# Kernel optimization log

Measured on AMD Instinct MI355X. Metric: run time of the kernel, lower is better.

Reference implementation:

```python
import jax, jax.numpy as jnp
import numpy as np

B, D, H, C = 32768, 512, 512, 128  # batch, input_dim, hidden, n_classes (nurse==doctor)
L = 3  # 3 PAN layers and 3 shared FC layers
BN_EPS = 1e-5


def setup_inputs() -> dict:
    key = jax.random.key(0)
    ks = iter(jax.random.split(key, 64))

    def rn(shape, scale):
        return (jax.random.normal(next(ks), shape, jnp.float32) * scale)

    inv = lambda fan: 1.0 / np.sqrt(fan)

    x = jax.random.normal(next(ks), (B, D), jnp.float32)
    s_n = jax.random.randint(next(ks), (B,), 0, C)
    s_d = jax.random.randint(next(ks), (B,), 0, C)
    # cols -4 / -3 carry integer staffing caps (s_nurse_max, s_doctor_max)
    x = x.at[:, -4].set(s_n.astype(jnp.float32)).at[:, -3].set(s_d.astype(jnp.float32))

    inp = {
        'x': x,
        # ClinicalPAN params, stacked over L=3 layers (and 3 branches)
        'pbw': rn((L, 3, D, 32), inv(D)), 'pbb': jnp.zeros((L, 3, 32), jnp.float32),
        'paw1': rn((L, D, 64), inv(D)),  'pab1': jnp.zeros((L, 64), jnp.float32),
        'paw2': rn((L, 64, 32), inv(64)),'pab2': jnp.zeros((L, 32), jnp.float32),
        'piw1': rn((L, D, 16), inv(D)),  'pib1': jnp.zeros((L, 16), jnp.float32),
        'piw2': rn((L, 16, 1), inv(16)), 'pib2': jnp.zeros((L, 1), jnp.float32),
        'pfw': rn((L, 96, D), inv(96)),  'pfb': jnp.zeros((L, D), jnp.float32),
        'pgw': rn((L, D, D), inv(D)),    'pgb': jnp.zeros((L, D), jnp.float32),
        # shared Linear + BatchNorm1d (eval mode: running stats), stacked
        'fcw': rn((L, D, H), inv(D)),    'fcb': jnp.zeros((L, H), jnp.float32),
        'bng': jnp.ones((L, H), jnp.float32),  'bnb': jnp.zeros((L, H), jnp.float32),
        'bnm': jnp.zeros((L, H), jnp.float32), 'bnv': jnp.ones((L, H), jnp.float32),
        # heads
        'nhw1': rn((H, 64), inv(H)), 'nhb1': jnp.zeros((64,), jnp.float32),
        'nhw2': rn((64, C), inv(64)), 'nhb2': jnp.zeros((C,), jnp.float32),
        'dhw1': rn((H, 64), inv(H)), 'dhb1': jnp.zeros((64,), jnp.float32),
        'dhw2': rn((64, C), inv(64)), 'dhb2': jnp.zeros((C,), jnp.float32),
        'wtw1': rn((H, 64), inv(H)), 'wtb1': jnp.zeros((64,), jnp.float32),
        'wtw2': rn((64, 1), inv(64)), 'wtb2': jnp.zeros((1,), jnp.float32),
    }
    return inp


def reference(x, pbw, pbb, paw1, pab1, paw2, pab2, piw1, pib1, piw2, pib2,
              pfw, pfb, pgw, pgb, fcw, fcb, bng, bnb, bnm, bnv,
              nhw1, nhb1, nhw2, nhb2, dhw1, dhb1, dhw2, dhb2,
              wtw1, wtb1, wtw2, wtb2):
    # integer caps (constants w.r.t. grad)
    s_n = jax.lax.stop_gradient(x[:, -4]).astype(jnp.int32)
    s_d = jax.lax.stop_gradient(x[:, -3]).astype(jnp.int32)

    h = x
    for l in range(L):  # ClinicalPAN stack (dropout = identity in eval)
        cw = jax.nn.sigmoid(jax.nn.relu(h @ paw1[l] + pab1[l]) @ paw2[l] + pab2[l])   # [B,32]
        ci = jax.nn.sigmoid(jax.nn.relu(h @ piw1[l] + pib1[l]) @ piw2[l] + pib2[l])   # [B,1]
        feats = jax.nn.relu(jnp.einsum('bd,kdh->bkh', h, pbw[l]) + pbb[l][None])      # [B,3,32]
        weighted = feats * (cw * ci)[:, None, :]                                       # [B,3,32]
        fused = weighted.reshape(h.shape[0], 96) @ pfw[l] + pfb[l]                     # [B,D]
        gate = jax.nn.sigmoid(h @ pgw[l] + pgb[l])
        h = fused + gate * h

    for i in range(L):  # shared Linear -> BN(eval) -> ReLU
        z = h @ fcw[i] + fcb[i]
        z = bng[i] * (z - bnm[i]) * jax.lax.rsqrt(bnv[i] + BN_EPS) + bnb[i]
        h = jax.nn.relu(z)

    nurse_logits = jax.nn.relu(h @ nhw1 + nhb1) @ nhw2 + nhb2   # [B,C]
    doctor_logits = jax.nn.relu(h @ dhw1 + dhb1) @ dhw2 + dhb2  # [B,C]
    wait_time = jax.nn.relu(h @ wtw1 + wtb1) @ wtw2 + wtb2      # [B,1]

    idx = jnp.arange(C)
    nm = (idx[None, :] <= s_n[:, None]).astype(nurse_logits.dtype)
    dm = (idx[None, :] <= s_d[:, None]).astype(doctor_logits.dtype)
    NEG = jnp.asarray(-1e9, nurse_logits.dtype)
    nurse_logits = nurse_logits * nm + (1.0 - nm) * NEG
    doctor_logits = doctor_logits * dm + (1.0 - dm) * NEG
    return nurse_logits, doctor_logits, wait_time
```

## Files before the change

kernel.cpp:

```cpp
#include <hip/hip_runtime.h>

#define DI __device__ __forceinline__

typedef short bf16x8 __attribute__((ext_vector_type(8)));
typedef float f32x4  __attribute__((ext_vector_type(4)));

#define MFMA(a,b,c) __builtin_amdgcn_mfma_f32_16x16x32_bf16(a,b,c,0,0,0)

constexpr int    SZ_WT = 512*80;
constexpr int    SZ_WB = 512*96;
constexpr int    SZ_WF = 96*512;
constexpr int    SZ_WG = 512*512;
constexpr int    SZ_WC = 512*512;
constexpr size_t OFF_WT  = 0;
constexpr size_t OFF_WB  = OFF_WT + 3*(size_t)SZ_WT;
constexpr size_t OFF_WF  = OFF_WB + 3*(size_t)SZ_WB;
constexpr size_t OFF_WG  = OFF_WF + 3*(size_t)SZ_WF;
constexpr size_t OFF_WC  = OFF_WG + 3*(size_t)SZ_WG;
constexpr size_t OFF_WH  = OFF_WC + 3*(size_t)SZ_WC;
constexpr size_t OFF_WH2 = OFF_WH + (size_t)512*192;
constexpr size_t WS_TOTAL= OFF_WH2 + (size_t)128*256;

DI short f2b(float f){ unsigned u; __builtin_memcpy(&u,&f,4); u += 0x7fffu + ((u>>16)&1u); return (short)(u>>16); }
DI float b2f(short s){ unsigned u = ((unsigned)(unsigned short)s)<<16; float f; __builtin_memcpy(&f,&u,4); return f; }
DI float sigm(float x){ return 1.f/(1.f+__expf(-x)); }
DI unsigned pk2(float a, float b){
  return (unsigned)(unsigned short)f2b(a) | ((unsigned)(unsigned short)f2b(b) << 16);
}

__global__ __launch_bounds__(256) void prep_weights(
    const float* __restrict__ pbw,  const float* __restrict__ paw1,
    const float* __restrict__ piw1, const float* __restrict__ pfw,
    const float* __restrict__ pgw,  const float* __restrict__ fcw,
    const float* __restrict__ nhw1, const float* __restrict__ nhw2,
    const float* __restrict__ dhw1, const float* __restrict__ dhw2,
    const float* __restrict__ wtw1, short* __restrict__ ws)
{
  size_t t = (size_t)blockIdx.x*256 + threadIdx.x;
  if (t >= WS_TOTAL) return;
  float v = 0.f;
  if (t < OFF_WB) {
    int q=(int)t; int ly=q/SZ_WT; int qq=q%SZ_WT;
    int j=qq&7, lane=(qq>>3)&63, tile=qq>>9, kt=tile&15, nt=tile>>4;
    int k=kt*32+((lane>>4)<<3)+j, n=nt*16+(lane&15);
    v = (n<64) ? paw1[((size_t)ly*512+k)*64+n] : piw1[((size_t)ly*512+k)*16+(n-64)];
  } else if (t < OFF_WF) {
    int q=(int)(t-OFF_WB); int ly=q/SZ_WB; int qq=q%SZ_WB;
    int j=qq&7, lane=(qq>>3)&63, tile=qq>>9, kt=tile&15, nt=tile>>4;
    int k=kt*32+((lane>>4)<<3)+j, c=nt*16+(lane&15);
    v = pbw[(((size_t)ly*3+(c>>5))*512+k)*32+(c&31)];
  } else if (t < OFF_WG) {
    int q=(int)(t-OFF_WF); int ly=q/SZ_WF; int qq=q%SZ_WF;
    int j=qq&7, lane=(qq>>3)&63, tile=qq>>9, kt=tile%3, nt=tile/3;
    int k=kt*32+((lane>>4)<<3)+j, n=nt*16+(lane&15);
    v = pfw[((size_t)ly*96+k)*512+n];
  } else if (t < OFF_WC) {
    int q=(int)(t-OFF_WG); int ly=q/SZ_WG; int qq=q%SZ_WG;
    int j=qq&7, lane=(qq>>3)&63, tile=qq>>9, kt=tile&15, nt=tile>>4;
    int k=kt*32+((lane>>4)<<3)+j, n=nt*16+(lane&15);
    v = pgw[((size_t)ly*512+k)*512+n];
  } else if (t < OFF_WH) {
    int q=(int)(t-OFF_WC); int ly=q/SZ_WC; int qq=q%SZ_WC;
    int j=qq&7, lane=(qq>>3)&63, tile=qq>>9, kt=tile&15, nt=tile>>4;
    int k=kt*32+((lane>>4)<<3)+j, n=nt*16+(lane&15);
    v = fcw[((size_t)ly*512+k)*512+n];
  } else if (t < OFF_WH2) {
    int qq=(int)(t-OFF_WH);
    int j=qq&7, lane=(qq>>3)&63, tile=qq>>9, kt=tile&15, nt=tile>>4;
    int k=kt*32+((lane>>4)<<3)+j, n=nt*16+(lane&15);
    v = (n<64) ? nhw1[(size_t)k*64+n] : (n<128) ? dhw1[(size_t)k*64+(n-64)] : wtw1[(size_t)k*64+(n-128)];
  } else {
    int qq=(int)(t-OFF_WH2);
    int j=qq&7, lane=(qq>>3)&63, tile=qq>>9, kt=tile&3, nt=tile>>2;
    int k=kt*32+((lane>>4)<<3)+j, n=nt*16+(lane&15);
    if (k<64) v = (n<128) ? nhw2[(size_t)k*128+n] : 0.f;
    else      v = (n>=128)? dhw2[(size_t)(k-64)*128+(n-128)] : 0.f;
  }
  ws[t] = f2b(v);
}

__global__ __launch_bounds__(512, 4) void pan_main(
  const float* __restrict__ x,
  const float* __restrict__ pbb,  const float* __restrict__ pab1,
  const float* __restrict__ paw2, const float* __restrict__ pab2,
  const float* __restrict__ pib1, const float* __restrict__ piw2,
  const float* __restrict__ pib2, const float* __restrict__ pfb,
  const float* __restrict__ pgb,  const float* __restrict__ fcb,
  const float* __restrict__ bng,  const float* __restrict__ bnb,
  const float* __restrict__ bnm,  const float* __restrict__ bnv,
  const float* __restrict__ nhb1, const float* __restrict__ nhb2,
  const float* __restrict__ dhb1, const float* __restrict__ dhb2,
  const float* __restrict__ wtb1, const float* __restrict__ wtw2,
  const float* __restrict__ wtb2,
  const short* __restrict__ ws, float* __restrict__ out)
{
  __shared__ __align__(16) char lds[81920];
  char* sH = lds;
  char* sU = lds + 65536;

  const int tid  = threadIdx.x;
  const int wave = tid >> 6;
  const int l    = tid & 63;
  const int lr   = l & 15;
  const int lb   = l >> 4;
  const int swzA = (lr & 7) << 4;
  const size_t row0 = (size_t)blockIdx.x * 64;

  #pragma unroll 2
  for (int c = tid; c < 4096; c += 512) {
    int row = c >> 6, k0 = (c & 63) << 3;
    const float4* s0 = (const float4*)(x + (row0 + row)*512 + k0);
    float4 f0 = s0[0], f1 = s0[1];
    bf16x8 p;
    p[0]=f2b(f0.x); p[1]=f2b(f0.y); p[2]=f2b(f0.z); p[3]=f2b(f0.w);
    p[4]=f2b(f1.x); p[5]=f2b(f1.y); p[6]=f2b(f1.z); p[7]=f2b(f1.w);
    *(bf16x8*)(sH + row*1024 + ((k0*2) ^ ((row&7)<<4))) = p;
  }
  __syncthreads();

  auto ldA = [&](int rt, int kt) -> bf16x8 {
    int row = rt*16 + lr;
    return *(const bf16x8*)(sH + row*1024 + ((kt*64 + lb*16) ^ swzA));
  };
  auto ldB = [&](const short* W, int K32, int nt, int kt) -> bf16x8 {
    return *(const bf16x8*)(W + (((size_t)(nt*K32 + kt))*64 + l)*8);
  };
  auto ldH = [&](int row, int col) -> float {
    return b2f(*(const short*)(sH + row*1024 + ((col*2) ^ ((row&7)<<4))));
  };
  const f32x4 FZ = {0.f,0.f,0.f,0.f};

  for (int ly = 0; ly < 3; ++ly) {
    if (wave < 5) {
      const short* W = ws + OFF_WT + (size_t)ly*SZ_WT;
      f32x4 acc[4];
      #pragma unroll
      for (int rt=0;rt<4;++rt) acc[rt] = FZ;
      #pragma unroll 2
      for (int kt=0;kt<16;++kt) {
        bf16x8 b = ldB(W,16,wave,kt);
        #pragma unroll
        for (int rt=0;rt<4;++rt) acc[rt] = MFMA(ldA(rt,kt), b, acc[rt]);
      }
      const int col = wave*16 + lr;
      const float bias = (col<64) ? pab1[ly*64+col] : pib1[ly*16+(col-64)];
      #pragma unroll
      for (int rt=0;rt<4;++rt)
        #pragma unroll
        for (int jj=0;jj<4;++jj) {
          int row = rt*16 + lb*4 + jj;
          *(short*)(sU + row*160 + col*2) = f2b(fmaxf(acc[rt][jj]+bias, 0.f));
        }
    }
    __syncthreads();
    if (tid < 64) {
      float s = pib2[ly];
      bf16x8 t0 = *(const bf16x8*)(sU + tid*160 + 128);
      bf16x8 t1 = *(const bf16x8*)(sU + tid*160 + 144);
      #pragma unroll
      for (int i=0;i<8;++i) {
        s += b2f(t0[i]) * piw2[ly*16+i];
        s += b2f(t1[i]) * piw2[ly*16+8+i];
      }
      *(float*)(sU + 10240 + tid*4) = sigm(s);
    }
    __syncthreads();
    {
      const int r = tid>>3, j0 = (tid&7)<<2;
      float a4[4];
      #pragma unroll
      for (int i=0;i<4;++i) a4[i] = pab2[ly*32 + j0 + i];
      #pragma unroll 2
      for (int k8=0;k8<8;++k8) {
        bf16x8 tv8 = *(const bf16x8*)(sU + r*160 + k8*16);
        #pragma unroll
        for (int i8=0;i8<8;++i8) {
          float tv = b2f(tv8[i8]);
          float4 wr = *(const float4*)(paw2 + ((size_t)ly*64 + k8*8+i8)*32 + j0);
          a4[0]=fmaf(tv,wr.x,a4[0]); a4[1]=fmaf(tv,wr.y,a4[1]);
          a4[2]=fmaf(tv,wr.z,a4[2]); a4[3]=fmaf(tv,wr.w,a4[3]);
        }
      }
      const float civ = *(const float*)(sU + 10240 + r*4);
      #pragma unroll
      for (int i=0;i<4;++i)
        *(short*)(sU + 10496 + (r*32 + j0 + i)*2) = f2b(sigm(a4[i]) * civ);
    }
    __syncthreads();
    unsigned wpk[4][2];
    if (wave < 6) {
      const short* W = ws + OFF_WB + (size_t)ly*SZ_WB;
      f32x4 acc[4];
      #pragma unroll
      for (int rt=0;rt<4;++rt) acc[rt] = FZ;
      #pragma unroll 2
      for (int kt=0;kt<16;++kt) {
        bf16x8 b = ldB(W,16,wave,kt);
        #pragma unroll
        for (int rt=0;rt<4;++rt) acc[rt] = MFMA(ldA(rt,kt), b, acc[rt]);
      }
      const int col = wave*16 + lr;
      const float bias = pbb[ly*96 + col];
      #pragma unroll
      for (int rt=0;rt<4;++rt) {
        float w4[4];
        #pragma unroll
        for (int jj=0;jj<4;++jj) {
          int row = rt*16 + lb*4 + jj;
          float cc = b2f(*(const short*)(sU + 10496 + (row*32 + (col&31))*2));
          w4[jj] = fmaxf(acc[rt][jj]+bias, 0.f) * cc;
        }
        wpk[rt][0] = pk2(w4[0], w4[1]);
        wpk[rt][1] = pk2(w4[2], w4[3]);
      }
    }
    __syncthreads();
    if (wave < 6) {
      const int col = wave*16 + lr;
      #pragma unroll
      for (int rt=0;rt<4;++rt)
        #pragma unroll
        for (int p=0;p<2;++p) {
          int r0 = rt*16 + lb*4 + p*2;
          unsigned v = wpk[rt][p];
          *(short*)(sU + r0*256     + ((col*2) ^ ((r0    &7)<<4))) = (short)(v & 0xffff);
          *(short*)(sU + (r0+1)*256 + ((col*2) ^ (((r0+1)&7)<<4))) = (short)(v >> 16);
        }
    }
    __syncthreads();
    unsigned pk[4][4][2];
    {
      const short* Wg = ws + OFF_WG + (size_t)ly*SZ_WG;
      const short* Wf = ws + OFF_WF + (size_t)ly*SZ_WF;
      #pragma unroll
      for (int p=0; p<2; ++p) {
        f32x4 acc[4][2];
        #pragma unroll
        for (int rt=0;rt<4;++rt) { acc[rt][0]=FZ; acc[rt][1]=FZ; }
        #pragma unroll 2
        for (int kt=0;kt<16;++kt) {
          bf16x8 b0 = ldB(Wg,16, wave*4+p*2+0, kt);
          bf16x8 b1 = ldB(Wg,16, wave*4+p*2+1, kt);
          #pragma unroll
          for (int rt=0;rt<4;++rt) {
            bf16x8 a = ldA(rt,kt);
            acc[rt][0] = MFMA(a,b0,acc[rt][0]);
            acc[rt][1] = MFMA(a,b1,acc[rt][1]);
          }
        }
        #pragma unroll
        for (int c2=0;c2<2;++c2) {
          const int col = (wave*4+p*2+c2)*16 + lr;
          const float gb = pgb[ly*512+col];
          const float fb = pfb[ly*512+col];
          #pragma unroll
          for (int rt=0;rt<4;++rt)
            #pragma unroll
            for (int jj=0;jj<4;++jj) {
              int row = rt*16 + lb*4 + jj;
              acc[rt][c2][jj] = sigm(acc[rt][c2][jj]+gb)*ldH(row,col) + fb;
            }
        }
        #pragma unroll 1
        for (int kt=0;kt<3;++kt) {
          bf16x8 b0 = ldB(Wf,3, wave*4+p*2+0, kt);
          bf16x8 b1 = ldB(Wf,3, wave*4+p*2+1, kt);
          #pragma unroll
          for (int rt=0;rt<4;++rt) {
            int row = rt*16 + lr;
            bf16x8 a = *(const bf16x8*)(sU + row*256 + ((kt*64 + lb*16) ^ swzA));
            acc[rt][0] = MFMA(a,b0,acc[rt][0]);
            acc[rt][1] = MFMA(a,b1,acc[rt][1]);
          }
        }
        #pragma unroll
        for (int c2=0;c2<2;++c2)
          #pragma unroll
          for (int rt=0;rt<4;++rt) {
            pk[p*2+c2][rt][0] = pk2(acc[rt][c2][0], acc[rt][c2][1]);
            pk[p*2+c2][rt][1] = pk2(acc[rt][c2][2], acc[rt][c2][3]);
          }
      }
    }
    __syncthreads();
    #pragma unroll
    for (int ci2=0;ci2<4;++ci2) {
      const int col = (wave*4+ci2)*16 + lr;
      #pragma unroll
      for (int rt=0;rt<4;++rt)
        #pragma unroll
        for (int q=0;q<2;++q) {
          int r0 = rt*16 + lb*4 + q*2;
          unsigned v = pk[ci2][rt][q];
          *(short*)(sH + r0*1024     + ((col*2) ^ ((r0    &7)<<4))) = (short)(v & 0xffff);
          *(short*)(sH + (r0+1)*1024 + ((col*2) ^ (((r0+1)&7)<<4))) = (short)(v >> 16);
        }
    }
    __syncthreads();
  }

  for (int fi=0; fi<3; ++fi) {
    const short* W = ws + OFF_WC + (size_t)fi*SZ_WC;
    unsigned pk[4][4][2];
    #pragma unroll
    for (int p=0; p<2; ++p) {
      f32x4 acc[4][2];
      #pragma unroll
      for (int rt=0;rt<4;++rt) { acc[rt][0]=FZ; acc[rt][1]=FZ; }
      #pragma unroll 2
      for (int kt=0;kt<16;++kt) {
        bf16x8 b0 = ldB(W,16, wave*4+p*2+0, kt);
        bf16x8 b1 = ldB(W,16, wave*4+p*2+1, kt);
        #pragma unroll
        for (int rt=0;rt<4;++rt) {
          bf16x8 a = ldA(rt,kt);
          acc[rt][0] = MFMA(a,b0,acc[rt][0]);
          acc[rt][1] = MFMA(a,b1,acc[rt][1]);
        }
      }
      #pragma unroll
      for (int c2=0;c2<2;++c2) {
        const int col = (wave*4+p*2+c2)*16 + lr;
        const float sc = bng[fi*512+col] * rsqrtf(bnv[fi*512+col] + 1e-5f);
        const float of = bnb[fi*512+col] - bnm[fi*512+col]*sc;
        const float bb = fcb[fi*512+col];
        #pragma unroll
        for (int rt=0;rt<4;++rt) {
          float z0 = fmaxf((acc[rt][c2][0] + bb)*sc + of, 0.f);
          float z1 = fmaxf((acc[rt][c2][1] + bb)*sc + of, 0.f);
          float z2 = fmaxf((acc[rt][c2][2] + bb)*sc + of, 0.f);
          float z3 = fmaxf((acc[rt][c2][3] + bb)*sc + of, 0.f);
          pk[p*2+c2][rt][0] = pk2(z0, z1);
          pk[p*2+c2][rt][1] = pk2(z2, z3);
        }
      }
    }
    __syncthreads();
    #pragma unroll
    for (int ci2=0;ci2<4;++ci2) {
      const int col = (wave*4+ci2)*16 + lr;
      #pragma unroll
      for (int rt=0;rt<4;++rt)
        #pragma unroll
        for (int q=0;q<2;++q) {
          int r0 = rt*16 + lb*4 + q*2;
          unsigned v = pk[ci2][rt][q];
          *(short*)(sH + r0*1024     + ((col*2) ^ ((r0    &7)<<4))) = (short)(v & 0xffff);
          *(short*)(sH + (r0+1)*1024 + ((col*2) ^ (((r0+1)&7)<<4))) = (short)(v >> 16);
        }
    }
    __syncthreads();
  }

  unsigned hkA[4][2], hkB[4][2];
  {
    const short* W = ws + OFF_WH;
    {
      f32x4 acc[4];
      #pragma unroll
      for (int rt=0;rt<4;++rt) acc[rt] = FZ;
      #pragma unroll 2
      for (int kt=0;kt<16;++kt) {
        bf16x8 b = ldB(W,16,wave,kt);
        #pragma unroll
        for (int rt=0;rt<4;++rt) acc[rt] = MFMA(ldA(rt,kt), b, acc[rt]);
      }
      const int col = wave*16 + lr;
      const float bias = (col<64) ? nhb1[col] : dhb1[col-64];
      #pragma unroll
      for (int rt=0;rt<4;++rt) {
        hkA[rt][0] = pk2(fmaxf(acc[rt][0]+bias,0.f), fmaxf(acc[rt][1]+bias,0.f));
        hkA[rt][1] = pk2(fmaxf(acc[rt][2]+bias,0.f), fmaxf(acc[rt][3]+bias,0.f));
      }
    }
    if (wave < 4) {
      f32x4 acc[4];
      #pragma unroll
      for (int rt=0;rt<4;++rt) acc[rt] = FZ;
      #pragma unroll 2
      for (int kt=0;kt<16;++kt) {
        bf16x8 b = ldB(W,16, 8+wave, kt);
        #pragma unroll
        for (int rt=0;rt<4;++rt) acc[rt] = MFMA(ldA(rt,kt), b, acc[rt]);
      }
      const int col = (8+wave)*16 + lr;
      const float bias = wtb1[col-128];
      #pragma unroll
      for (int rt=0;rt<4;++rt) {
        hkB[rt][0] = pk2(fmaxf(acc[rt][0]+bias,0.f), fmaxf(acc[rt][1]+bias,0.f));
        hkB[rt][1] = pk2(fmaxf(acc[rt][2]+bias,0.f), fmaxf(acc[rt][3]+bias,0.f));
      }
    }
  }
  __syncthreads();
  {
    #pragma unroll
    for (int rt=0;rt<4;++rt)
      #pragma unroll
      for (int q=0;q<2;++q) {
        int r0 = rt*16 + lb*4 + q*2;
        int cA = wave*16 + lr;
        unsigned v = hkA[rt][q];
        *(short*)(lds + r0*384     + ((cA*2) ^ ((r0    &7)<<4))) = (short)(v & 0xffff);
        *(short*)(lds + (r0+1)*384 + ((cA*2) ^ (((r0+1)&7)<<4))) = (short)(v >> 16);
      }
    if (wave < 4) {
      #pragma unroll
      for (int rt=0;rt<4;++rt)
        #pragma unroll
        for (int q=0;q<2;++q) {
          int r0 = rt*16 + lb*4 + q*2;
          int cB = (8+wave)*16 + lr;
          unsigned v = hkB[rt][q];
          *(short*)(lds + r0*384     + ((cB*2) ^ ((r0    &7)<<4))) = (short)(v & 0xffff);
          *(short*)(lds + (r0+1)*384 + ((cB*2) ^ (((r0+1)&7)<<4))) = (short)(v >> 16);
        }
    }
  }
  __syncthreads();
  {
    const short* W2 = ws + OFF_WH2;
    #pragma unroll
    for (int p=0;p<2;++p) {
      f32x4 acc[4];
      #pragma unroll
      for (int rt=0;rt<4;++rt) acc[rt] = FZ;
      #pragma unroll 2
      for (int kt=0;kt<4;++kt) {
        bf16x8 b = ldB(W2,4, wave*2+p, kt);
        #pragma unroll
        for (int rt=0;rt<4;++rt) {
          int row = rt*16 + lr;
          bf16x8 a = *(const bf16x8*)(lds + row*384 + ((kt*64 + lb*16) ^ swzA));
          acc[rt] = MFMA(a,b,acc[rt]);
        }
      }
      const int col2 = (wave*2+p)*16 + lr;
      const bool isn = col2 < 128;
      const int cc = col2 & 127;
      const float bias = isn ? nhb2[cc] : dhb2[cc];
      const size_t obase = isn ? (size_t)0 : (size_t)4194304;
      #pragma unroll
      for (int rt=0;rt<4;++rt)
        #pragma unroll
        for (int jj=0;jj<4;++jj) {
          int row = rt*16 + lb*4 + jj;
          size_t rg = row0 + row;
          float2 caps = *(const float2*)(x + rg*512 + 508);
          int cap = (int)(isn ? caps.x : caps.y);
          float v = acc[rt][jj] + bias;
          out[obase + rg*128 + cc] = (cc <= cap) ? v : -1e9f;
        }
    }
  }
  if (tid < 64) {
    float s = wtb2[0];
    #pragma unroll 2
    for (int k8=0;k8<8;++k8) {
      bf16x8 hv = *(const bf16x8*)(lds + tid*384 + ((256 + k8*16) ^ ((tid&7)<<4)));
      #pragma unroll
      for (int i=0;i<8;++i) s += b2f(hv[i]) * wtw2[k8*8+i];
    }
    out[(size_t)8388608 + row0 + tid] = s;
  }
}

extern "C" void kernel_launch(void* const* d_in, const int* in_sizes, int n_in,
                              void* d_out, int out_size, void* d_ws, size_t ws_size,
                              hipStream_t stream) {
  const float* x    = (const float*)d_in[0];
  const float* pbw  = (const float*)d_in[1];
  const float* pbb  = (const float*)d_in[2];
  const float* paw1 = (const float*)d_in[3];
  const float* pab1 = (const float*)d_in[4];
  const float* paw2 = (const float*)d_in[5];
  const float* pab2 = (const float*)d_in[6];
  const float* piw1 = (const float*)d_in[7];
  const float* pib1 = (const float*)d_in[8];
  const float* piw2 = (const float*)d_in[9];
  const float* pib2 = (const float*)d_in[10];
  const float* pfw  = (const float*)d_in[11];
  const float* pfb  = (const float*)d_in[12];
  const float* pgw  = (const float*)d_in[13];
  const float* pgb  = (const float*)d_in[14];
  const float* fcw  = (const float*)d_in[15];
  const float* fcb  = (const float*)d_in[16];
  const float* bng  = (const float*)d_in[17];
  const float* bnb  = (const float*)d_in[18];
  const float* bnm  = (const float*)d_in[19];
  const float* bnv  = (const float*)d_in[20];
  const float* nhw1 = (const float*)d_in[21];
  const float* nhb1 = (const float*)d_in[22];
  const float* nhw2 = (const float*)d_in[23];
  const float* nhb2 = (const float*)d_in[24];
  const float* dhw1 = (const float*)d_in[25];
  const float* dhb1 = (const float*)d_in[26];
  const float* dhw2 = (const float*)d_in[27];
  const float* dhb2 = (const float*)d_in[28];
  const float* wtw1 = (const float*)d_in[29];
  const float* wtb1 = (const float*)d_in[30];
  const float* wtw2 = (const float*)d_in[31];
  const float* wtb2 = (const float*)d_in[32];
  short* ws  = (short*)d_ws;
  float* out = (float*)d_out;

  prep_weights<<<(int)((WS_TOTAL + 255)/256), 256, 0, stream>>>(
      pbw, paw1, piw1, pfw, pgw, fcw, nhw1, nhw2, dhw1, dhw2, wtw1, ws);
  pan_main<<<512, 512, 0, stream>>>(
      x, pbb, pab1, paw2, pab2, pib1, piw2, pib2, pfb, pgb, fcb,
      bng, bnb, bnm, bnv, nhb1, nhb2, dhb1, dhb2, wtb1, wtw2, wtb2, ws, out);
}
```

Before: 330.1 us.

## Ping-pong hidden state between two LDS buffers to drop register staging and barriers

Adds a second 64 KB LDS buffer for the hidden state so each layer writes its output straight into the other buffer, then swaps pointers. This removes the pack-into-registers step and the extra `__syncthreads` pairs that previously guarded in-place overwrites of a single buffer. The weighted-branch features and head activations are likewise written directly to LDS. In exchange, LDS per block roughly doubles to 160 KB and the launch bound is relaxed to 2 blocks per SM. That likely allows only one 512-thread block per CU, cutting occupancy and latency hiding.

Result: slower. 356.3 us (+7.9%).

```diff
diff --git a/kernel.cpp b/kernel.cpp
--- a/kernel.cpp
+++ b/kernel.cpp
@@ -24,9 +24,6 @@
 DI short f2b(float f){ unsigned u; __builtin_memcpy(&u,&f,4); u += 0x7fffu + ((u>>16)&1u); return (short)(u>>16); }
 DI float b2f(short s){ unsigned u = ((unsigned)(unsigned short)s)<<16; float f; __builtin_memcpy(&f,&u,4); return f; }
 DI float sigm(float x){ return 1.f/(1.f+__expf(-x)); }
-DI unsigned pk2(float a, float b){
-  return (unsigned)(unsigned short)f2b(a) | ((unsigned)(unsigned short)f2b(b) << 16);
-}
 
 __global__ __launch_bounds__(256) void prep_weights(
     const float* __restrict__ pbw,  const float* __restrict__ paw1,
@@ -79,7 +76,7 @@
   ws[t] = f2b(v);
 }
 
-__global__ __launch_bounds__(512, 4) void pan_main(
+__global__ __launch_bounds__(512, 2) void pan_main(
   const float* __restrict__ x,
   const float* __restrict__ pbb,  const float* __restrict__ pab1,
   const float* __restrict__ paw2, const float* __restrict__ pab2,
@@ -94,9 +91,11 @@
   const float* __restrict__ wtb2,
   const short* __restrict__ ws, float* __restrict__ out)
 {
-  __shared__ __align__(16) char lds[81920];
-  char* sH = lds;
-  char* sU = lds + 65536;
+  __shared__ __align__(16) char lds[163840];
+  char* hA = lds;
+  char* hB = lds + 65536;
+  char* sU = lds + 131072;
+  char* sW = lds + 147456;
 
   const int tid  = threadIdx.x;
   const int wave = tid >> 6;
@@ -114,19 +113,22 @@
     bf16x8 p;
     p[0]=f2b(f0.x); p[1]=f2b(f0.y); p[2]=f2b(f0.z); p[3]=f2b(f0.w);
     p[4]=f2b(f1.x); p[5]=f2b(f1.y); p[6]=f2b(f1.z); p[7]=f2b(f1.w);
-    *(bf16x8*)(sH + row*1024 + ((k0*2) ^ ((row&7)<<4))) = p;
+    *(bf16x8*)(hA + row*1024 + ((k0*2) ^ ((row&7)<<4))) = p;
   }
   __syncthreads();
 
-  auto ldA = [&](int rt, int kt) -> bf16x8 {
+  auto ldA = [&](const char* base, int rt, int kt) -> bf16x8 {
     int row = rt*16 + lr;
-    return *(const bf16x8*)(sH + row*1024 + ((kt*64 + lb*16) ^ swzA));
+    return *(const bf16x8*)(base + row*1024 + ((kt*64 + lb*16) ^ swzA));
   };
   auto ldB = [&](const short* W, int K32, int nt, int kt) -> bf16x8 {
     return *(const bf16x8*)(W + (((size_t)(nt*K32 + kt))*64 + l)*8);
   };
-  auto ldH = [&](int row, int col) -> float {
-    return b2f(*(const short*)(sH + row*1024 + ((col*2) ^ ((row&7)<<4))));
+  auto ldH = [&](const char* base, int row, int col) -> float {
+    return b2f(*(const short*)(base + row*1024 + ((col*2) ^ ((row&7)<<4))));
+  };
+  auto stH = [&](char* base, int row, int col, float v) {
+    *(short*)(base + row*1024 + ((col*2) ^ ((row&7)<<4))) = f2b(v);
   };
   const f32x4 FZ = {0.f,0.f,0.f,0.f};
 
@@ -140,7 +142,7 @@
       for (int kt=0;kt<16;++kt) {
         bf16x8 b = ldB(W,16,wave,kt);
         #pragma unroll
-        for (int rt=0;rt<4;++rt) acc[rt] = MFMA(ldA(rt,kt), b, acc[rt]);
+        for (int rt=0;rt<4;++rt) acc[rt] = MFMA(ldA(hA,rt,kt), b, acc[rt]);
       }
       const int col = wave*16 + lr;
       const float bias = (col<64) ? pab1[ly*64+col] : pib1[ly*16+(col-64)];
@@ -187,7 +189,6 @@
         *(short*)(sU + 10496 + (r*32 + j0 + i)*2) = f2b(sigm(a4[i]) * civ);
     }
     __syncthreads();
-    unsigned wpk[4][2];
     if (wave < 6) {
       const short* W = ws + OFF_WB + (size_t)ly*SZ_WB;
       f32x4 acc[4];
@@ -197,38 +198,21 @@
       for (int kt=0;kt<16;++kt) {
         bf16x8 b = ldB(W,16,wave,kt);
         #pragma unroll
-        for (int rt=0;rt<4;++rt) acc[rt] = MFMA(ldA(rt,kt), b, acc[rt]);
+        for (int rt=0;rt<4;++rt) acc[rt] = MFMA(ldA(hA,rt,kt), b, acc[rt]);
       }
       const int col = wave*16 + lr;
       const float bias = pbb[ly*96 + col];
       #pragma unroll
-      for (int rt=0;rt<4;++rt) {
-        float w4[4];
+      for (int rt=0;rt<4;++rt)
         #pragma unroll
         for (int jj=0;jj<4;++jj) {
           int row = rt*16 + lb*4 + jj;
           float cc = b2f(*(const short*)(sU + 10496 + (row*32 + (col&31))*2));
-          w4[jj] = fmaxf(acc[rt][jj]+bias, 0.f) * cc;
-        }
-        wpk[rt][0] = pk2(w4[0], w4[1]);
-        wpk[rt][1] = pk2(w4[2], w4[3]);
-      }
-    }
-    __syncthreads();
-    if (wave < 6) {
-      const int col = wave*16 + lr;
-      #pragma unroll
-      for (int rt=0;rt<4;++rt)
-        #pragma unroll
-        for (int p=0;p<2;++p) {
-          int r0 = rt*16 + lb*4 + p*2;
-          unsigned v = wpk[rt][p];
-          *(short*)(sU + r0*256     + ((col*2) ^ ((r0    &7)<<4))) = (short)(v & 0xffff);
-          *(short*)(sU + (r0+1)*256 + ((col*2) ^ (((r0+1)&7)<<4))) = (short)(v >> 16);
-        }
-    }
-    __syncthreads();
-    unsigned pk[4][4][2];
+          float wv = fmaxf(acc[rt][jj]+bias, 0.f) * cc;
+          *(short*)(sW + row*256 + ((col*2) ^ ((row&7)<<4))) = f2b(wv);
+        }
+    }
+    __syncthreads();
     {
       const short* Wg = ws + OFF_WG + (size_t)ly*SZ_WG;
       const short* Wf = ws + OFF_WF + (size_t)ly*SZ_WF;
@@ -243,7 +227,7 @@
           bf16x8 b1 = ldB(Wg,16, wave*4+p*2+1, kt);
           #pragma unroll
           for (int rt=0;rt<4;++rt) {
-            bf16x8 a = ldA(rt,kt);
+            bf16x8 a = ldA(hA,rt,kt);
             acc[rt][0] = MFMA(a,b0,acc[rt][0]);
             acc[rt][1] = MFMA(a,b1,acc[rt][1]);
           }
@@ -258,7 +242,7 @@
             #pragma unroll
             for (int jj=0;jj<4;++jj) {
               int row = rt*16 + lb*4 + jj;
-              acc[rt][c2][jj] = sigm(acc[rt][c2][jj]+gb)*ldH(row,col) + fb;
+              acc[rt][c2][jj] = sigm(acc[rt][c2][jj]+gb)*ldH(hA,row,col) + fb;
             }
         }
         #pragma unroll 1
@@ -268,40 +252,28 @@
           #pragma unroll
           for (int rt=0;rt<4;++rt) {
             int row = rt*16 + lr;
-            bf16x8 a = *(const bf16x8*)(sU + row*256 + ((kt*64 + lb*16) ^ swzA));
+            bf16x8 a = *(const bf16x8*)(sW + row*256 + ((kt*64 + lb*16) ^ swzA));
             acc[rt][0] = MFMA(a,b0,acc[rt][0]);
             acc[rt][1] = MFMA(a,b1,acc[rt][1]);
           }
         }
         #pragma unroll
-        for (int c2=0;c2<2;++c2)
+        for (int c2=0;c2<2;++c2) {
+          const int col = (wave*4+p*2+c2)*16 + lr;
           #pragma unroll
-          for (int rt=0;rt<4;++rt) {
-            pk[p*2+c2][rt][0] = pk2(acc[rt][c2][0], acc[rt][c2][1]);
-            pk[p*2+c2][rt][1] = pk2(acc[rt][c2][2], acc[rt][c2][3]);
-          }
-      }
-    }
-    __syncthreads();
-    #pragma unroll
-    for (int ci2=0;ci2<4;++ci2) {
-      const int col = (wave*4+ci2)*16 + lr;
-      #pragma unroll
-      for (int rt=0;rt<4;++rt)
-        #pragma unroll
-        for (int q=0;q<2;++q) {
-          int r0 = rt*16 + lb*4 + q*2;
-          unsigned v = pk[ci2][rt][q];
-          *(short*)(sH + r0*1024     + ((col*2) ^ ((r0    &7)<<4))) = (short)(v & 0xffff);
-          *(short*)(sH + (r0+1)*1024 + ((col*2) ^ (((r0+1)&7)<<4))) = (short)(v >> 16);
-        }
-    }
-    __syncthreads();
+          for (int rt=0;rt<4;++rt)
+            #pragma unroll
+            for (int jj=0;jj<4;++jj)
+              stH(hB, rt*16 + lb*4 + jj, col, acc[rt][c2][jj]);
+        }
+      }
+    }
+    __syncthreads();
+    { char* t = hA; hA = hB; hB = t; }
   }
 
   for (int fi=0; fi<3; ++fi) {
     const short* W = ws + OFF_WC + (size_t)fi*SZ_WC;
-    unsigned pk[4][4][2];
     #pragma unroll
     for (int p=0; p<2; ++p) {
       f32x4 acc[4][2];
@@ -313,7 +285,7 @@
         bf16x8 b1 = ldB(W,16, wave*4+p*2+1, kt);
         #pragma unroll
         for (int rt=0;rt<4;++rt) {
-          bf16x8 a = ldA(rt,kt);
+          bf16x8 a = ldA(hA,rt,kt);
           acc[rt][0] = MFMA(a,b0,acc[rt][0]);
           acc[rt][1] = MFMA(a,b1,acc[rt][1]);
         }
@@ -325,34 +297,17 @@
         const float of = bnb[fi*512+col] - bnm[fi*512+col]*sc;
         const float bb = fcb[fi*512+col];
         #pragma unroll
-        for (int rt=0;rt<4;++rt) {
-          float z0 = fmaxf((acc[rt][c2][0] + bb)*sc + of, 0.f);
-          float z1 = fmaxf((acc[rt][c2][1] + bb)*sc + of, 0.f);
-          float z2 = fmaxf((acc[rt][c2][2] + bb)*sc + of, 0.f);
-          float z3 = fmaxf((acc[rt][c2][3] + bb)*sc + of, 0.f);
-          pk[p*2+c2][rt][0] = pk2(z0, z1);
-          pk[p*2+c2][rt][1] = pk2(z2, z3);
-        }
-      }
-    }
-    __syncthreads();
-    #pragma unroll
-    for (int ci2=0;ci2<4;++ci2) {
-      const int col = (wave*4+ci2)*16 + lr;
-      #pragma unroll
-      for (int rt=0;rt<4;++rt)
-        #pragma unroll
-        for (int q=0;q<2;++q) {
-          int r0 = rt*16 + lb*4 + q*2;
-          unsigned v = pk[ci2][rt][q];
-          *(short*)(sH + r0*1024     + ((col*2) ^ ((r0    &7)<<4))) = (short)(v & 0xffff);
-          *(short*)(sH + (r0+1)*1024 + ((col*2) ^ (((r0+1)&7)<<4))) = (short)(v >> 16);
-        }
-    }
-    __syncthreads();
-  }
-
-  unsigned hkA[4][2], hkB[4][2];
+        for (int rt=0;rt<4;++rt)
+          #pragma unroll
+          for (int jj=0;jj<4;++jj)
+            stH(hB, rt*16 + lb*4 + jj, col,
+                fmaxf((acc[rt][c2][jj] + bb)*sc + of, 0.f));
+      }
+    }
+    __syncthreads();
+    { char* t = hA; hA = hB; hB = t; }
+  }
+
   {
     const short* W = ws + OFF_WH;
     {
@@ -363,15 +318,18 @@
       for (int kt=0;kt<16;++kt) {
         bf16x8 b = ldB(W,16,wave,kt);
         #pragma unroll
-        for (int rt=0;rt<4;++rt) acc[rt] = MFMA(ldA(rt,kt), b, acc[rt]);
+        for (int rt=0;rt<4;++rt) acc[rt] = MFMA(ldA(hA,rt,kt), b, acc[rt]);
       }
       const int col = wave*16 + lr;
       const float bias = (col<64) ? nhb1[col] : dhb1[col-64];
       #pragma unroll
-      for (int rt=0;rt<4;++rt) {
-        hkA[rt][0] = pk2(fmaxf(acc[rt][0]+bias,0.f), fmaxf(acc[rt][1]+bias,0.f));
-        hkA[rt][1] = pk2(fmaxf(acc[rt][2]+bias,0.f), fmaxf(acc[rt][3]+bias,0.f));
-      }
+      for (int rt=0;rt<4;++rt)
+        #pragma unroll
+        for (int jj=0;jj<4;++jj) {
+          int row = rt*16 + lb*4 + jj;
+          *(short*)(hB + row*384 + ((col*2) ^ ((row&7)<<4))) =
+              f2b(fmaxf(acc[rt][jj]+bias, 0.f));
+        }
     }
     if (wave < 4) {
       f32x4 acc[4];
@@ -381,39 +339,17 @@
       for (int kt=0;kt<16;++kt) {
         bf16x8 b = ldB(W,16, 8+wave, kt);
         #pragma unroll
-        for (int rt=0;rt<4;++rt) acc[rt] = MFMA(ldA(rt,kt), b, acc[rt]);
+        for (int rt=0;rt<4;++rt) acc[rt] = MFMA(ldA(hA,rt,kt), b, acc[rt]);
       }
       const int col = (8+wave)*16 + lr;
       const float bias = wtb1[col-128];
       #pragma unroll
-      for (int rt=0;rt<4;++rt) {
-        hkB[rt][0] = pk2(fmaxf(acc[rt][0]+bias,0.f), fmaxf(acc[rt][1]+bias,0.f));
-        hkB[rt][1] = pk2(fmaxf(acc[rt][2]+bias,0.f), fmaxf(acc[rt][3]+bias,0.f));
-      }
-    }
-  }
-  __syncthreads();
-  {
-    #pragma unroll
-    for (int rt=0;rt<4;++rt)
-      #pragma unroll
-      for (int q=0;q<2;++q) {
-        int r0 = rt*16 + lb*4 + q*2;
-        int cA = wave*16 + lr;
-        unsigned v = hkA[rt][q];
-        *(short*)(lds + r0*384     + ((cA*2) ^ ((r0    &7)<<4))) = (short)(v & 0xffff);
-        *(short*)(lds + (r0+1)*384 + ((cA*2) ^ (((r0+1)&7)<<4))) = (short)(v >> 16);
-      }
-    if (wave < 4) {
-      #pragma unroll
       for (int rt=0;rt<4;++rt)
         #pragma unroll
-        for (int q=0;q<2;++q) {
-          int r0 = rt*16 + lb*4 + q*2;
-          int cB = (8+wave)*16 + lr;
-          unsigned v = hkB[rt][q];
-          *(short*)(lds + r0*384     + ((cB*2) ^ ((r0    &7)<<4))) = (short)(v & 0xffff);
-          *(short*)(lds + (r0+1)*384 + ((cB*2) ^ (((r0+1)&7)<<4))) = (short)(v >> 16);
+        for (int jj=0;jj<4;++jj) {
+          int row = rt*16 + lb*4 + jj;
+          *(short*)(hB + row*384 + ((col*2) ^ ((row&7)<<4))) =
+              f2b(fmaxf(acc[rt][jj]+bias, 0.f));
         }
     }
   }
@@ -431,7 +367,7 @@
         #pragma unroll
         for (int rt=0;rt<4;++rt) {
           int row = rt*16 + lr;
-          bf16x8 a = *(const bf16x8*)(lds + row*384 + ((kt*64 + lb*16) ^ swzA));
+          bf16x8 a = *(const bf16x8*)(hB + row*384 + ((kt*64 + lb*16) ^ swzA));
           acc[rt] = MFMA(a,b,acc[rt]);
         }
       }
@@ -457,7 +393,7 @@
     float s = wtb2[0];
     #pragma unroll 2
     for (int k8=0;k8<8;++k8) {
-      bf16x8 hv = *(const bf16x8*)(lds + tid*384 + ((256 + k8*16) ^ ((tid&7)<<4)));
+      bf16x8 hv = *(const bf16x8*)(hB + tid*384 + ((256 + k8*16) ^ ((tid&7)<<4)));
       #pragma unroll
       for (int i=0;i<8;++i) s += b2f(hv[i]) * wtw2[k8*8+i];
     }
```
